# Kernel tuning notes

Measured on AMD Instinct MI355X. Metric: run time of the kernel, lower is better.

Reference implementation:

```python
import jax, jax.numpy as jnp
import numpy as np

N = 4096        # active agents (all active)
H = 64          # hidden_dim
L = 3           # GAT layers
AVG_DEG = 32.0
NEG_SLOPE = 0.2  # PyG GATConv default
EPS = 1e-5       # layer_norm eps


def setup_inputs() -> dict:
    key = jax.random.key(0)
    ks = jax.random.split(key, 12)
    # binary compatibility graph with ~AVG_DEG in/out degree
    adjacency_matrix = (jax.random.uniform(ks[0], (N, N)) < AVG_DEG / N).astype(jnp.float32)
    arrivals = jax.random.uniform(ks[1], (N,), dtype=jnp.float32) * 4.0
    departures = arrivals + 1.0 + jax.random.uniform(ks[2], (N,), dtype=jnp.float32) * 8.0
    is_hard_to_match = (jax.random.uniform(ks[3], (N,)) < 0.5).astype(jnp.float32)
    active_agents = jnp.ones((N,), dtype=jnp.float32)  # all active (see notes)
    s = 1.0 / np.sqrt(H)
    return dict(
        adjacency_matrix=adjacency_matrix,
        timestep=5,
        arrivals=arrivals,
        departures=departures,
        is_hard_to_match=is_hard_to_match,
        active_agents=active_agents,
        emb_w1=jax.random.normal(ks[4], (2, H), dtype=jnp.float32) * 0.5,
        emb_b1=jnp.zeros((H,), jnp.float32),
        emb_w2=jax.random.normal(ks[5], (H, H), dtype=jnp.float32) * s,
        emb_b2=jnp.zeros((H,), jnp.float32),
        gat_w=jax.random.normal(ks[6], (L, H, H), dtype=jnp.float32) * s,
        gat_asrc=jax.random.normal(ks[7], (L, H), dtype=jnp.float32) * s,
        gat_adst=jax.random.normal(ks[8], (L, H), dtype=jnp.float32) * s,
        gat_b=jnp.zeros((L, H), jnp.float32),
        val_w=jax.random.normal(ks[9], (H, 1), dtype=jnp.float32) * s,
        val_b=jnp.zeros((1,), jnp.float32),
    )


def reference(adjacency_matrix, timestep, arrivals, departures, is_hard_to_match,
              active_agents, emb_w1, emb_b1, emb_w2, emb_b2,
              gat_w, gat_asrc, gat_adst, gat_b, val_w, val_b):
    n = adjacency_matrix.shape[0]
    # mask[i, j] = True if edge j -> i exists (edge_index row0 = src row of adj),
    # plus self-loops (PyG GATConv add_self_loops=True)
    mask = (adjacency_matrix.T != 0) | jnp.eye(n, dtype=bool)

    # node features: progress through stay + hard-to-match flag  -> [N, 2]
    progress = (timestep - arrivals) / (departures - arrivals)
    feat = jnp.stack([progress, is_hard_to_match], axis=1)
    # embedding = two stacked Linears, NO nonlinearity between them
    x = (feat @ emb_w1 + emb_b1) @ emb_w2 + emb_b2  # [N, H]

    # GAT (heads=1): ReLU between layers, none after the last
    h = x
    for l in range(L):
        hw = h @ gat_w[l]                                   # [N, H]
        e = jax.nn.leaky_relu((hw @ gat_asrc[l])[None, :]   # src score per col j
                              + (hw @ gat_adst[l])[:, None],  # dst score per row i
                              NEG_SLOPE)                    # [N, N], e[i, j] edge j->i
        alpha = jax.nn.softmax(jnp.where(mask, e, -jnp.inf), axis=1)
        h = alpha @ hw + gat_b[l]
        if l < L - 1:
            h = jax.nn.relu(h)

    x = x + h
    # F.layer_norm over feature dim, no affine
    mu = jnp.mean(x, axis=-1, keepdims=True)
    var = jnp.mean((x - mu) ** 2, axis=-1, keepdims=True)
    x = (x - mu) / jnp.sqrt(var + EPS)

    pooled = jnp.mean(x, axis=0)                            # global_mean_pool, 1 graph
    out = jax.nn.relu(pooled @ val_w + val_b)               # [1]
    return out.squeeze()
```

## Files before the change

kernel.cpp:

```cpp
#include <hip/hip_runtime.h>
#include <math.h>

#define N 4096
#define NB 128
#define BANDSZ 32
#define MAXDEG 128
#define NEG_SLOPE 0.2f
#define LN_EPS 1e-5f

__device__ __forceinline__ float wave_reduce_sum(float v) {
    #pragma unroll
    for (int m = 32; m >= 1; m >>= 1) v += __shfl_xor(v, m, 64);
    return v;
}
__device__ __forceinline__ float wave_reduce_max(float v) {
    #pragma unroll
    for (int m = 32; m >= 1; m >>= 1) v = fmaxf(v, __shfl_xor(v, m, 64));
    return v;
}

__device__ __forceinline__ float transform_row(float hv, const float* __restrict__ W,
                                               int lane) {
    float tr = 0.f;
    #pragma unroll
    for (int k = 0; k < 64; ++k)
        tr += __shfl(hv, k, 64) * W[k * 64 + lane];
    return tr;
}

__device__ __forceinline__ float agg_core(int j0, int j1, int deg, float sd,
        const float* __restrict__ ssin, const float* __restrict__ hwin,
        const float* __restrict__ b, int lane) {
    float e0 = -1e30f, e1 = -1e30f;
    if (lane < deg)      { float v = ssin[j0] + sd; e0 = v > 0.f ? v : NEG_SLOPE * v; }
    if (lane + 64 < deg) { float v = ssin[j1] + sd; e1 = v > 0.f ? v : NEG_SLOPE * v; }
    float m = wave_reduce_max(fmaxf(e0, e1));
    float p0 = (lane < deg)      ? expf(e0 - m) : 0.f;
    float p1 = (lane + 64 < deg) ? expf(e1 - m) : 0.f;
    float Z = wave_reduce_sum(p0 + p1);
    float acc = 0.f;
    int d0 = min(deg, 64);
    #pragma unroll 4
    for (int n = 0; n < d0; ++n) {
        int   jj = __shfl(j0, n, 64);
        float p  = __shfl(p0, n, 64);
        acc += p * hwin[jj * 64 + lane];
    }
    for (int n = 64; n < deg; ++n) {
        int   jj = __shfl(j1, n - 64, 64);
        float p  = __shfl(p1, n - 64, 64);
        acc += p * hwin[jj * 64 + lane];
    }
    return acc / Z + b[lane];
}

__device__ __forceinline__ float agg_half(int j0, int j1, int deg, float sd,
        const float* __restrict__ ssin, const float* __restrict__ hwin,
        int lane, int lo, int hi, float* Zout) {
    float e0 = -1e30f, e1 = -1e30f;
    if (lane < deg)      { float v = ssin[j0] + sd; e0 = v > 0.f ? v : NEG_SLOPE * v; }
    if (lane + 64 < deg) { float v = ssin[j1] + sd; e1 = v > 0.f ? v : NEG_SLOPE * v; }
    float m = wave_reduce_max(fmaxf(e0, e1));
    float p0 = (lane < deg)      ? expf(e0 - m) : 0.f;
    float p1 = (lane + 64 < deg) ? expf(e1 - m) : 0.f;
    *Zout = wave_reduce_sum(p0 + p1);
    float acc = 0.f;
    int hi0 = min(hi, 64);
    #pragma unroll 4
    for (int n = lo; n < hi0; ++n) {
        int   jj = __shfl(j0, n, 64);
        float p  = __shfl(p0, n, 64);
        acc += p * hwin[jj * 64 + lane];
    }
    #pragma unroll 2
    for (int n = (lo > 64 ? lo : 64); n < hi; ++n) {
        int   jj = __shfl(j1, n - 64, 64);
        float p  = __shfl(p1, n - 64, 64);
        acc += p * hwin[jj * 64 + lane];
    }
    return acc;
}

__global__ void __launch_bounds__(256) prep_kernel(
        const float4* __restrict__ adj4, const int* __restrict__ timestep,
        const float* __restrict__ arr, const float* __restrict__ dep,
        const float* __restrict__ hard,
        const float* __restrict__ w1, const float* __restrict__ b1,
        const float* __restrict__ w2, const float* __restrict__ b2,
        const float* __restrict__ W0, const float* __restrict__ asrc,
        const float* __restrict__ adst,
        uint4* __restrict__ bm4,
        float* __restrict__ x, float* __restrict__ hwA,
        float* __restrict__ ssA, float* __restrict__ sdA,
        float* __restrict__ accum, int* __restrict__ done) {
    int wave = threadIdx.x >> 6;
    int lane = threadIdx.x & 63;
    if (blockIdx.x < 512) {
        int t    = blockIdx.x * 256 + threadIdx.x;
        int cg   = t & 1023;
        int band = t >> 10;
        int jbase = band * BANDSZ;
        unsigned m0 = 0u, m1 = 0u, m2 = 0u, m3 = 0u;
        #pragma unroll
        for (int batch = 0; batch < 4; ++batch) {
            float4 a[8];
            #pragma unroll
            for (int u = 0; u < 8; ++u)
                a[u] = adj4[(size_t)(jbase + batch * 8 + u) * 1024 + cg];
            #pragma unroll
            for (int u = 0; u < 8; ++u) {
                unsigned bit = batch * 8 + u;
                m0 |= (unsigned)(a[u].x != 0.f) << bit;
                m1 |= (unsigned)(a[u].y != 0.f) << bit;
                m2 |= (unsigned)(a[u].z != 0.f) << bit;
                m3 |= (unsigned)(a[u].w != 0.f) << bit;
            }
        }
        uint4 m; m.x = m0; m.y = m1; m.z = m2; m.w = m3;
        bm4[band * 1024 + cg] = m;
        if (blockIdx.x == 0 && threadIdx.x == 0) { *accum = 0.f; *done = 0; }
    } else {
        int row = (blockIdx.x - 512) * 4 + wave;
        float ts = (float)(*timestep);
        float pr = (ts - arr[row]) / (dep[row] - arr[row]);
        float hd = hard[row];
        float t  = pr * w1[lane] + hd * w1[64 + lane] + b1[lane];
        float xv = b2[lane];
        #pragma unroll
        for (int k = 0; k < 64; ++k)
            xv += __shfl(t, k, 64) * w2[k * 64 + lane];
        x[row * 64 + lane] = xv;
        float tr = transform_row(xv, W0, lane);
        hwA[row * 64 + lane] = tr;
        float s1 = wave_reduce_sum(tr * asrc[lane]);
        float s2 = wave_reduce_sum(tr * adst[lane]);
        if (lane == 0) { ssA[row] = s1; sdA[row] = s2; }
    }
}

__global__ void __launch_bounds__(256) compact_agg_tr(
        const unsigned* __restrict__ bm,
        const float* __restrict__ hwin, const float* __restrict__ ssin,
        const float* __restrict__ sdin, const float* __restrict__ b,
        const float* __restrict__ W, const float* __restrict__ asrc,
        const float* __restrict__ adst,
        int* __restrict__ nbr_c, int* __restrict__ deg_arr,
        float* __restrict__ hwout, float* __restrict__ ssout,
        float* __restrict__ sdout) {
    __shared__ int lds[4][MAXDEG];
    int wave = threadIdx.x >> 6;
    int lane = threadIdx.x & 63;
    int i = blockIdx.x * 4 + wave;
    unsigned m0 = bm[(2 * lane)     * N + i];
    unsigned m1 = bm[(2 * lane + 1) * N + i];
    int selfband = i >> 5;
    if (2 * lane     == selfband) m0 |= 1u << (i & 31);
    if (2 * lane + 1 == selfband) m1 |= 1u << (i & 31);
    int c0 = __popc(m0);
    int c1 = __popc(m1);
    int c  = c0 + c1;
    int inc = c;
    #pragma unroll
    for (int s = 1; s < 64; s <<= 1) {
        int t = __shfl_up(inc, s, 64);
        if (lane >= s) inc += t;
    }
    int off = inc - c;
    int deg = min(__shfl(inc, 63, 64), MAXDEG);
    {
        int o = off;
        unsigned mm = m0; int base = (2 * lane) * 32;
        while (mm) { int bit = __ffs(mm) - 1; mm &= mm - 1;
                     if (o < MAXDEG) lds[wave][o] = base + bit; ++o; }
        mm = m1; base = (2 * lane + 1) * 32;
        while (mm) { int bit = __ffs(mm) - 1; mm &= mm - 1;
                     if (o < MAXDEG) lds[wave][o] = base + bit; ++o; }
    }
    __syncthreads();
    int j0 = (lane < deg)      ? lds[wave][lane]      : 0;
    int j1 = (lane + 64 < deg) ? lds[wave][lane + 64] : 0;
    if (lane < deg)      nbr_c[i * MAXDEG + lane]      = j0;
    if (lane + 64 < deg) nbr_c[i * MAXDEG + lane + 64] = j1;
    if (lane == 0) deg_arr[i] = deg;
    float hv = fmaxf(agg_core(j0, j1, deg, sdin[i], ssin, hwin, b, lane), 0.f);
    float tr = transform_row(hv, W, lane);
    hwout[i * 64 + lane] = tr;
    float s1 = wave_reduce_sum(tr * asrc[lane]);
    float s2 = wave_reduce_sum(tr * adst[lane]);
    if (lane == 0) { ssout[i] = s1; sdout[i] = s2; }
}

__global__ void __launch_bounds__(512, 8) agg_tr(
        const float* __restrict__ hwin, const float* __restrict__ ssin,
        const float* __restrict__ sdin, const int* __restrict__ nbr_c,
        const int* __restrict__ deg_arr, const float* __restrict__ b,
        const float* __restrict__ W, const float* __restrict__ asrc,
        const float* __restrict__ adst,
        float* __restrict__ hwout, float* __restrict__ ssout,
        float* __restrict__ sdout) {
    __shared__ float accb[4][64];
    int w    = threadIdx.x >> 6;
    int lane = threadIdx.x & 63;
    int r    = w >> 1;
    int half = w & 1;
    int i = blockIdx.x * 4 + r;
    int deg = deg_arr[i];
    int j0 = (lane < deg)      ? nbr_c[i * MAXDEG + lane]      : 0;
    int j1 = (lane + 64 < deg) ? nbr_c[i * MAXDEG + lane + 64] : 0;
    int h  = (deg + 1) >> 1;
    float Z;
    float acc = agg_half(j0, j1, deg, sdin[i], ssin, hwin, lane,
                         half ? h : 0, half ? deg : h, &Z);
    if (half) accb[r][lane] = acc;
    __syncthreads();
    if (!half) {
        acc += accb[r][lane];
        float hv = fmaxf(acc / Z + b[lane], 0.f);
        float tr = transform_row(hv, W, lane);
        hwout[i * 64 + lane] = tr;
        float s1 = wave_reduce_sum(tr * asrc[lane]);
        float s2 = wave_reduce_sum(tr * adst[lane]);
        if (lane == 0) { ssout[i] = s1; sdout[i] = s2; }
    }
}

__global__ void __launch_bounds__(512, 8) agg_final_finish(
        const float* __restrict__ hwin, const float* __restrict__ ssin,
        const float* __restrict__ sdin, const int* __restrict__ nbr_c,
        const int* __restrict__ deg_arr, const float* __restrict__ b,
        const float* __restrict__ x, const float* __restrict__ vw,
        const float* __restrict__ vb,
        float* __restrict__ accum, int* __restrict__ done,
        float* __restrict__ out) {
    __shared__ float accb[4][64];
    __shared__ float sp[4];
    int w    = threadIdx.x >> 6;
    int lane = threadIdx.x & 63;
    int r    = w >> 1;
    int half = w & 1;
    int i = blockIdx.x * 4 + r;
    int deg = deg_arr[i];
    int j0 = (lane < deg)      ? nbr_c[i * MAXDEG + lane]      : 0;
    int j1 = (lane + 64 < deg) ? nbr_c[i * MAXDEG + lane + 64] : 0;
    int h  = (deg + 1) >> 1;
    float Z;
    float acc = agg_half(j0, j1, deg, sdin[i], ssin, hwin, lane,
                         half ? h : 0, half ? deg : h, &Z);
    if (half) accb[r][lane] = acc;
    __syncthreads();
    if (!half) {
        acc += accb[r][lane];
        float hv = acc / Z + b[lane];
        float v  = x[i * 64 + lane] + hv;
        float mu = wave_reduce_sum(v) * (1.f / 64.f);
        float d  = v - mu;
        float var = wave_reduce_sum(d * d) * (1.f / 64.f);
        float ln  = d * rsqrtf(var + LN_EPS);
        float part = wave_reduce_sum(ln * vw[lane]);
        if (lane == 0) sp[r] = part;
    }
    __syncthreads();
    if (threadIdx.x == 0) {
        float bp = sp[0] + sp[1] + sp[2] + sp[3];
        atomicAdd(accum, bp);
        __threadfence();
        int old = atomicAdd(done, 1);
        if (old == (N / 4) - 1) {
            float t = __hip_atomic_load(accum, __ATOMIC_RELAXED,
                                        __HIP_MEMORY_SCOPE_AGENT);
            out[0] = fmaxf(t * (1.f / (float)N) + vb[0], 0.f);
        }
    }
}

extern "C" void kernel_launch(void* const* d_in, const int* in_sizes, int n_in,
                              void* d_out, int out_size, void* d_ws, size_t ws_size,
                              hipStream_t stream) {
    const float4* adj4      = (const float4*)d_in[0];
    const int*   timestep   = (const int*)  d_in[1];
    const float* arrivals   = (const float*)d_in[2];
    const float* departures = (const float*)d_in[3];
    const float* hard       = (const float*)d_in[4];
    const float* emb_w1     = (const float*)d_in[6];
    const float* emb_b1     = (const float*)d_in[7];
    const float* emb_w2     = (const float*)d_in[8];
    const float* emb_b2     = (const float*)d_in[9];
    const float* gat_w      = (const float*)d_in[10];
    const float* gat_asrc   = (const float*)d_in[11];
    const float* gat_adst   = (const float*)d_in[12];
    const float* gat_b      = (const float*)d_in[13];
    const float* val_w      = (const float*)d_in[14];
    const float* val_b      = (const float*)d_in[15];

    const size_t MB = 1u << 20;
    char* ws = (char*)d_ws;
    unsigned* bm   = (unsigned*)(ws);
    int*   nbr_c   = (int*)  (ws + 4 * MB);
    int*   deg_arr = (int*)  (ws + 6 * MB);
    float* x       = (float*)(ws + 7 * MB);
    float* hwA     = (float*)(ws + 8 * MB);
    float* hwB     = (float*)(ws + 9 * MB);
    float* ssA     = (float*)(ws + 10 * MB);
    float* sdA     = (float*)(ws + 10 * MB + 65536);
    float* ssB     = (float*)(ws + 10 * MB + 131072);
    float* sdB     = (float*)(ws + 10 * MB + 196608);
    float* accum   = (float*)(ws + 11 * MB);
    int*   done    = (int*)  (ws + 11 * MB + 64);

    prep_kernel<<<1536, 256, 0, stream>>>(adj4, timestep, arrivals, departures, hard,
                                          emb_w1, emb_b1, emb_w2, emb_b2,
                                          gat_w, gat_asrc, gat_adst,
                                          (uint4*)bm, x, hwA, ssA, sdA, accum, done);
    compact_agg_tr<<<N / 4, 256, 0, stream>>>(bm, hwA, ssA, sdA, gat_b,
                                              gat_w + 64 * 64, gat_asrc + 64,
                                              gat_adst + 64,
                                              nbr_c, deg_arr, hwB, ssB, sdB);
    agg_tr<<<N / 4, 512, 0, stream>>>(hwB, ssB, sdB, nbr_c, deg_arr, gat_b + 64,
                                      gat_w + 2 * 64 * 64, gat_asrc + 128,
                                      gat_adst + 128, hwA, ssA, sdA);
    agg_final_finish<<<N / 4, 512, 0, stream>>>(hwA, ssA, sdA, nbr_c, deg_arr,
                                                gat_b + 128, x, val_w, val_b,
                                                accum, done, (float*)d_out);
    (void)in_sizes; (void)n_in; (void)out_size; (void)ws_size;
}
```

Baseline: 186.1 us.

## Transpose bitmask layout and split first-layer aggregation across two waves per row

The prep kernel now writes the adjacency bitmask transposed (row-major by destination node), so the compaction kernel reads each row's 128 band words as one contiguous uint2 per lane instead of strided loads. The first compact+aggregate kernel moves to 512 threads, with two waves per row each aggregating half the neighbours and combining the partial sums through shared memory, matching the later layers. The gather loop unroll goes from 4 to 8. In exchange, the bitmask stores in prep become scattered 4-byte writes, and the extra waves redundantly recompute the compaction and softmax.

```diff
diff --git a/kernel.cpp b/kernel.cpp
--- a/kernel.cpp
+++ b/kernel.cpp
@@ -26,32 +26,6 @@
     for (int k = 0; k < 64; ++k)
         tr += __shfl(hv, k, 64) * W[k * 64 + lane];
     return tr;
-}
-
-__device__ __forceinline__ float agg_core(int j0, int j1, int deg, float sd,
-        const float* __restrict__ ssin, const float* __restrict__ hwin,
-        const float* __restrict__ b, int lane) {
-    float e0 = -1e30f, e1 = -1e30f;
-    if (lane < deg)      { float v = ssin[j0] + sd; e0 = v > 0.f ? v : NEG_SLOPE * v; }
-    if (lane + 64 < deg) { float v = ssin[j1] + sd; e1 = v > 0.f ? v : NEG_SLOPE * v; }
-    float m = wave_reduce_max(fmaxf(e0, e1));
-    float p0 = (lane < deg)      ? expf(e0 - m) : 0.f;
-    float p1 = (lane + 64 < deg) ? expf(e1 - m) : 0.f;
-    float Z = wave_reduce_sum(p0 + p1);
-    float acc = 0.f;
-    int d0 = min(deg, 64);
-    #pragma unroll 4
-    for (int n = 0; n < d0; ++n) {
-        int   jj = __shfl(j0, n, 64);
-        float p  = __shfl(p0, n, 64);
-        acc += p * hwin[jj * 64 + lane];
-    }
-    for (int n = 64; n < deg; ++n) {
-        int   jj = __shfl(j1, n - 64, 64);
-        float p  = __shfl(p1, n - 64, 64);
-        acc += p * hwin[jj * 64 + lane];
-    }
-    return acc / Z + b[lane];
 }
 
 __device__ __forceinline__ float agg_half(int j0, int j1, int deg, float sd,
@@ -66,7 +40,7 @@
     *Zout = wave_reduce_sum(p0 + p1);
     float acc = 0.f;
     int hi0 = min(hi, 64);
-    #pragma unroll 4
+    #pragma unroll 8
     for (int n = lo; n < hi0; ++n) {
         int   jj = __shfl(j0, n, 64);
         float p  = __shfl(p0, n, 64);
@@ -89,7 +63,7 @@
         const float* __restrict__ w2, const float* __restrict__ b2,
         const float* __restrict__ W0, const float* __restrict__ asrc,
         const float* __restrict__ adst,
-        uint4* __restrict__ bm4,
+        unsigned* __restrict__ bmT,
         float* __restrict__ x, float* __restrict__ hwA,
         float* __restrict__ ssA, float* __restrict__ sdA,
         float* __restrict__ accum, int* __restrict__ done) {
@@ -99,6 +73,7 @@
         int t    = blockIdx.x * 256 + threadIdx.x;
         int cg   = t & 1023;
         int band = t >> 10;
+        int i0   = cg * 4;
         int jbase = band * BANDSZ;
         unsigned m0 = 0u, m1 = 0u, m2 = 0u, m3 = 0u;
         #pragma unroll
@@ -116,8 +91,10 @@
                 m3 |= (unsigned)(a[u].w != 0.f) << bit;
             }
         }
-        uint4 m; m.x = m0; m.y = m1; m.z = m2; m.w = m3;
-        bm4[band * 1024 + cg] = m;
+        bmT[(i0 + 0) * NB + band] = m0;
+        bmT[(i0 + 1) * NB + band] = m1;
+        bmT[(i0 + 2) * NB + band] = m2;
+        bmT[(i0 + 3) * NB + band] = m3;
         if (blockIdx.x == 0 && threadIdx.x == 0) { *accum = 0.f; *done = 0; }
     } else {
         int row = (blockIdx.x - 512) * 4 + wave;
@@ -138,8 +115,8 @@
     }
 }
 
-__global__ void __launch_bounds__(256) compact_agg_tr(
-        const unsigned* __restrict__ bm,
+__global__ void __launch_bounds__(512, 8) compact_agg_tr(
+        const unsigned* __restrict__ bmT,
         const float* __restrict__ hwin, const float* __restrict__ ssin,
         const float* __restrict__ sdin, const float* __restrict__ b,
         const float* __restrict__ W, const float* __restrict__ asrc,
@@ -148,11 +125,14 @@
         float* __restrict__ hwout, float* __restrict__ ssout,
         float* __restrict__ sdout) {
     __shared__ int lds[4][MAXDEG];
-    int wave = threadIdx.x >> 6;
+    __shared__ float accb[4][64];
+    int w    = threadIdx.x >> 6;
     int lane = threadIdx.x & 63;
-    int i = blockIdx.x * 4 + wave;
-    unsigned m0 = bm[(2 * lane)     * N + i];
-    unsigned m1 = bm[(2 * lane + 1) * N + i];
+    int r    = w >> 1;
+    int half = w & 1;
+    int i = blockIdx.x * 4 + r;
+    uint2 mv = *(const uint2*)(bmT + i * NB + 2 * lane);
+    unsigned m0 = mv.x, m1 = mv.y;
     int selfband = i >> 5;
     if (2 * lane     == selfband) m0 |= 1u << (i & 31);
     if (2 * lane + 1 == selfband) m1 |= 1u << (i & 31);
@@ -171,23 +151,34 @@
         int o = off;
         unsigned mm = m0; int base = (2 * lane) * 32;
         while (mm) { int bit = __ffs(mm) - 1; mm &= mm - 1;
-                     if (o < MAXDEG) lds[wave][o] = base + bit; ++o; }
+                     if (o < MAXDEG) lds[r][o] = base + bit; ++o; }
         mm = m1; base = (2 * lane + 1) * 32;
         while (mm) { int bit = __ffs(mm) - 1; mm &= mm - 1;
-                     if (o < MAXDEG) lds[wave][o] = base + bit; ++o; }
-    }
-    __syncthreads();
-    int j0 = (lane < deg)      ? lds[wave][lane]      : 0;
-    int j1 = (lane + 64 < deg) ? lds[wave][lane + 64] : 0;
-    if (lane < deg)      nbr_c[i * MAXDEG + lane]      = j0;
-    if (lane + 64 < deg) nbr_c[i * MAXDEG + lane + 64] = j1;
-    if (lane == 0) deg_arr[i] = deg;
-    float hv = fmaxf(agg_core(j0, j1, deg, sdin[i], ssin, hwin, b, lane), 0.f);
-    float tr = transform_row(hv, W, lane);
-    hwout[i * 64 + lane] = tr;
-    float s1 = wave_reduce_sum(tr * asrc[lane]);
-    float s2 = wave_reduce_sum(tr * adst[lane]);
-    if (lane == 0) { ssout[i] = s1; sdout[i] = s2; }
+                     if (o < MAXDEG) lds[r][o] = base + bit; ++o; }
+    }
+    __syncthreads();
+    int j0 = (lane < deg)      ? lds[r][lane]      : 0;
+    int j1 = (lane + 64 < deg) ? lds[r][lane + 64] : 0;
+    if (!half) {
+        if (lane < deg)      nbr_c[i * MAXDEG + lane]      = j0;
+        if (lane + 64 < deg) nbr_c[i * MAXDEG + lane + 64] = j1;
+        if (lane == 0) deg_arr[i] = deg;
+    }
+    int h = (deg + 1) >> 1;
+    float Z;
+    float acc = agg_half(j0, j1, deg, sdin[i], ssin, hwin, lane,
+                         half ? h : 0, half ? deg : h, &Z);
+    if (half) accb[r][lane] = acc;
+    __syncthreads();
+    if (!half) {
+        acc += accb[r][lane];
+        float hv = fmaxf(acc / Z + b[lane], 0.f);
+        float tr = transform_row(hv, W, lane);
+        hwout[i * 64 + lane] = tr;
+        float s1 = wave_reduce_sum(tr * asrc[lane]);
+        float s2 = wave_reduce_sum(tr * adst[lane]);
+        if (lane == 0) { ssout[i] = s1; sdout[i] = s2; }
+    }
 }
 
 __global__ void __launch_bounds__(512, 8) agg_tr(
@@ -294,7 +285,7 @@
 
     const size_t MB = 1u << 20;
     char* ws = (char*)d_ws;
-    unsigned* bm   = (unsigned*)(ws);
+    unsigned* bmT  = (unsigned*)(ws);
     int*   nbr_c   = (int*)  (ws + 4 * MB);
     int*   deg_arr = (int*)  (ws + 6 * MB);
     float* x       = (float*)(ws + 7 * MB);
@@ -310,8 +301,8 @@
     prep_kernel<<<1536, 256, 0, stream>>>(adj4, timestep, arrivals, departures, hard,
                                           emb_w1, emb_b1, emb_w2, emb_b2,
                                           gat_w, gat_asrc, gat_adst,
-                                          (uint4*)bm, x, hwA, ssA, sdA, accum, done);
-    compact_agg_tr<<<N / 4, 256, 0, stream>>>(bm, hwA, ssA, sdA, gat_b,
+                                          bmT, x, hwA, ssA, sdA, accum, done);
+    compact_agg_tr<<<N / 4, 512, 0, stream>>>(bmT, hwA, ssA, sdA, gat_b,
                                               gat_w + 64 * 64, gat_asrc + 64,
                                               gat_adst + 64,
                                               nbr_c, deg_arr, hwB, ssB, sdB);
```

New measurement: 186.9 us. About the same (+0.4%).
